# Kernel tuning notes

Hardware: AMD Instinct MI355X
Metric: run time of the kernel (lower is better)

## Reference

```python
import jax, jax.numpy as jnp
import numpy as np

DIM = 1536
NUM_HEADS = 16
HEAD_DIM = DIM // NUM_HEADS  # 96
ROPE_DIM = HEAD_DIM // 2     # 48
PT_SEQ = 32
FT_SEQ = 32
EPS = 1e-6


def _rope_tables():
    # VisionRotaryEmbedding(dim=48, pt_seq_len=32): 2D axial rotary tables
    f = 1.0 / (10000.0 ** (np.arange(0, ROPE_DIM, 2, dtype=np.float32)[: ROPE_DIM // 2] / ROPE_DIM))
    pos = np.arange(FT_SEQ, dtype=np.float32) / FT_SEQ * PT_SEQ
    freqs = pos[:, None] * f[None, :]                       # [32, 24]
    freqs = np.repeat(freqs, 2, axis=-1)                    # [32, 48] interleaved
    row = np.broadcast_to(freqs[:, None, :], (FT_SEQ, FT_SEQ, ROPE_DIM))
    col = np.broadcast_to(freqs[None, :, :], (FT_SEQ, FT_SEQ, ROPE_DIM))
    grid = np.concatenate([row, col], axis=-1).reshape(-1, HEAD_DIM)  # [1024, 96]
    return jnp.asarray(np.cos(grid)), jnp.asarray(np.sin(grid))


def _apply_rotary(x, cos, sin):
    # x: [B, S, H, D]; cos/sin: [S, D]; interleaved (use_real_unbind_dim=-1) rotation
    xr = x.reshape(*x.shape[:-1], -1, 2)
    x_rot = jnp.stack([-xr[..., 1], xr[..., 0]], axis=-1).reshape(x.shape)
    return x * cos[None, :, None, :] + x_rot * sin[None, :, None, :]


def _rms_norm(x, w):
    var = jnp.mean(jnp.square(x), axis=-1, keepdims=True)
    return x * jax.lax.rsqrt(var + EPS) * w


def setup_inputs() -> dict:
    key = jax.random.key(0)
    ks = jax.random.split(key, 12)
    s = 1.0 / np.sqrt(DIM)
    return {
        "hidden_states": jax.random.normal(ks[0], (8, 1024, DIM), dtype=jnp.float32),
        "Wq": jax.random.normal(ks[1], (DIM, DIM), dtype=jnp.float32) * s,
        "bq": jax.random.normal(ks[2], (DIM,), dtype=jnp.float32) * 0.01,
        "Wk": jax.random.normal(ks[3], (DIM, DIM), dtype=jnp.float32) * s,
        "bk": jax.random.normal(ks[4], (DIM,), dtype=jnp.float32) * 0.01,
        "Wv": jax.random.normal(ks[5], (DIM, DIM), dtype=jnp.float32) * s,
        "bv": jax.random.normal(ks[6], (DIM,), dtype=jnp.float32) * 0.01,
        "q_norm_w": jnp.ones((HEAD_DIM,), dtype=jnp.float32),
        "k_norm_w": jnp.ones((HEAD_DIM,), dtype=jnp.float32),
        "Wo": jax.random.normal(ks[7], (DIM, DIM), dtype=jnp.float32) * s,
        "bo": jax.random.normal(ks[8], (DIM,), dtype=jnp.float32) * 0.01,
    }


def reference(hidden_states, Wq, bq, Wk, bk, Wv, bv, q_norm_w, k_norm_w, Wo, bo):
    B, S, _ = hidden_states.shape
    cos, sin = _rope_tables()  # [S, HEAD_DIM], constants

    q = hidden_states @ Wq.T + bq
    k = hidden_states @ Wk.T + bk
    v = hidden_states @ Wv.T + bv
    q = q.reshape(B, S, NUM_HEADS, HEAD_DIM)
    k = k.reshape(B, S, NUM_HEADS, HEAD_DIM)
    v = v.reshape(B, S, NUM_HEADS, HEAD_DIM)

    q = _rms_norm(q, q_norm_w)
    k = _rms_norm(k, k_norm_w)
    q = _apply_rotary(q, cos, sin)
    k = _apply_rotary(k, cos, sin)

    scale = 1.0 / np.sqrt(HEAD_DIM)
    scores = jnp.einsum("bshd,bthd->bhst", q, k) * scale  # [B, H, S, S]
    probs = jax.nn.softmax(scores, axis=-1)
    out = jnp.einsum("bhst,bthd->bshd", probs, v)          # [B, S, H, D]
    out = out.reshape(B, S, DIM)
    return out @ Wo.T + bo
```

## Files before the change

kernel.cpp:

```cpp
#include <hip/hip_runtime.h>
#include <hip/hip_bf16.h>
#include <math.h>

typedef __hip_bfloat16 bf16;
typedef __attribute__((ext_vector_type(8))) short short8;
typedef __attribute__((ext_vector_type(4))) short short4v;
typedef __attribute__((ext_vector_type(4))) float f32x4;
typedef __attribute__((ext_vector_type(2))) int int2v;

#define MFMA16(a, b, c) __builtin_amdgcn_mfma_f32_16x16x32_bf16((a), (b), (c), 0, 0, 0)

typedef const __attribute__((address_space(1))) void GVOID;
typedef __attribute__((address_space(3))) void LVOID;

__device__ __forceinline__ float b2f(short s) {
    union { unsigned u; float f; } v;
    v.u = ((unsigned)(unsigned short)s) << 16;
    return v.f;
}
__device__ __forceinline__ short f2b(float f) {
    union { float f; unsigned u; } v;
    v.f = f;
    unsigned r = v.u + 0x7fffu + ((v.u >> 16) & 1u);
    return (short)(r >> 16);
}
__device__ __forceinline__ unsigned packbf2(float a, float b) {
    float2 t; t.x = a; t.y = b;
    __hip_bfloat162 h = __float22bfloat162_rn(t);
    union { __hip_bfloat162 h; unsigned u; } cv; cv.h = h;
    return cv.u;
}
__device__ __forceinline__ short bf2s(float x) {
    __hip_bfloat16 h = __float2bfloat16(x);
    union { __hip_bfloat16 h; short s; } cv; cv.h = h;
    return cv.s;
}

#if __has_builtin(__builtin_amdgcn_permlane32_swap)
__device__ __forceinline__ float addx32(float x) {
    union { float f; int i; } c; c.f = x;
    int2v r = __builtin_amdgcn_permlane32_swap(c.i, c.i, false, false);
    union { int i; float f; } a, b; a.i = r[0]; b.i = r[1];
    return a.f + b.f;
}
__device__ __forceinline__ float maxx32(float x) {
    union { float f; int i; } c; c.f = x;
    int2v r = __builtin_amdgcn_permlane32_swap(c.i, c.i, false, false);
    union { int i; float f; } a, b; a.i = r[0]; b.i = r[1];
    return fmaxf(a.f, b.f);
}
#else
__device__ __forceinline__ float addx32(float x) { return x + __shfl_xor(x, 32); }
__device__ __forceinline__ float maxx32(float x) { return fmaxf(x, __shfl_xor(x, 32)); }
#endif

#if __has_builtin(__builtin_amdgcn_permlane16_swap)
__device__ __forceinline__ float addx16(float x) {
    union { float f; int i; } c; c.f = x;
    int2v r = __builtin_amdgcn_permlane16_swap(c.i, c.i, false, false);
    union { int i; float f; } a, b; a.i = r[0]; b.i = r[1];
    return a.f + b.f;
}
__device__ __forceinline__ float maxx16(float x) {
    union { float f; int i; } c; c.f = x;
    int2v r = __builtin_amdgcn_permlane16_swap(c.i, c.i, false, false);
    union { int i; float f; } a, b; a.i = r[0]; b.i = r[1];
    return fmaxf(a.f, b.f);
}
#else
__device__ __forceinline__ float addx16(float x) { return x + __shfl_xor(x, 16); }
__device__ __forceinline__ float maxx16(float x) { return fmaxf(x, __shfl_xor(x, 16)); }
#endif

__global__ __launch_bounds__(256) void prep_kernel(
    const unsigned* __restrict__ X,
    const void* __restrict__ bq, const void* __restrict__ bk,
    const void* __restrict__ bv, const void* __restrict__ bo,
    const void* __restrict__ qw, const void* __restrict__ kw,
    int* __restrict__ flag, float* __restrict__ biasqkv, float* __restrict__ boc,
    float* __restrict__ qwc, float* __restrict__ kwc,
    float* __restrict__ cosT, float* __restrict__ sinT)
{
    const int tid = threadIdx.x;
    if (blockIdx.x == 0) {
        __shared__ int cnt;
        if (tid == 0) cnt = 0;
        __syncthreads();
        unsigned w = X[tid];
        unsigned e = (w >> 7) & 0xFFu;
        if (e > 140u) atomicAdd(&cnt, 1);
        __syncthreads();
        const int f = (cnt >= 16) ? 1 : 0;
        if (tid == 0) *flag = f;
        for (int i = tid; i < 6336; i += 256) {
            const void* src; float* dst; int j;
            if (i < 4608) {
                int m = i / 1536; j = i - m * 1536;
                src = (m == 0) ? bq : (m == 1) ? bk : bv; dst = biasqkv + i;
            } else if (i < 6144) { j = i - 4608; src = bo; dst = boc + j; }
            else if (i < 6240)   { j = i - 6144; src = qw; dst = qwc + j; }
            else                 { j = i - 6240; src = kw; dst = kwc + j; }
            *dst = f ? ((const float*)src)[j] : b2f(((const short*)src)[j]);
        }
    } else {
        int idx = (blockIdx.x - 1) * 256 + tid;
        if (idx >= 1024 * 96) return;
        int p = idx / 96;
        int d = idx - p * 96;
        int r = p >> 5, c = p & 31;
        int inRow = (d < 48);
        int dd = inRow ? d : d - 48;
        float pos = inRow ? (float)r : (float)c;
        float ex = -(float)(dd & ~1) / 48.0f;
        float f = powf(10000.0f, ex);
        float ang = pos * f;
        cosT[idx] = cosf(ang);
        sinT[idx] = sinf(ang);
    }
}

__device__ __forceinline__ void canon8(const void* src, short* dst, int i, int f) {
    short8 o;
    if (f) {
        const float* s = (const float*)src + (size_t)i * 8;
#pragma unroll
        for (int j = 0; j < 8; ++j) o[j] = f2b(s[j]);
    } else {
        o = ((const short8*)src)[i];
    }
    ((short8*)dst)[i] = o;
}

__global__ __launch_bounds__(256) void canon_all_kernel(
    const void* __restrict__ X,
    const void* __restrict__ s0, const void* __restrict__ s1,
    const void* __restrict__ s2, const void* __restrict__ s3,
    short* __restrict__ dX,
    short* __restrict__ d0, short* __restrict__ d1,
    short* __restrict__ d2, short* __restrict__ d3,
    const int* __restrict__ flag)
{
    const int f = *flag;
    const int bid = blockIdx.x;
    if (bid < 6144) {
        canon8(X, dX, bid * 256 + threadIdx.x, f);
    } else {
        const int wb = bid - 6144;
        const int m = wb / 1152;
        const int i = (wb - m * 1152) * 256 + threadIdx.x;
        const void* src = (m == 0) ? s0 : (m == 1) ? s1 : (m == 2) ? s2 : s3;
        short* dst = (m == 0) ? d0 : (m == 1) ? d1 : (m == 2) ? d2 : d3;
        canon8(src, dst, i, f);
    }
}

__global__ __launch_bounds__(256) void gemm128_kernel(
    const bf16* __restrict__ A, const bf16* __restrict__ Bw,
    const float* __restrict__ bias,
    bf16* __restrict__ O0, bf16* __restrict__ O1, bf16* __restrict__ O2,
    int K, const int* __restrict__ outFlag)
{
    __shared__ __align__(16) short As[2][128 * 64];
    __shared__ __align__(16) short Bs[2][128 * 64];

    const int tid = threadIdx.x;
    const int lane = tid & 63, w = tid >> 6;
    const int wr = w >> 1, wc = w & 1;
    const int li = lane & 15, lg = lane >> 4;

    const int pp = blockIdx.y * gridDim.x + blockIdx.x;
    const int xcd = pp & 7;
    const int idx = pp >> 3;
    const int mb = xcd * 8 + (idx & 7);
    const int nb = idx >> 3;
    const long mBase = (long)mb * 128;
    const long nGlob = (long)nb * 128;

    const bf16* aSrc[4]; const bf16* bSrc[4]; int ldsOff[4];
#pragma unroll
    for (int u = 0; u < 4; ++u) {
        const int L = u * 4096 + tid * 16;
        const int S = L ^ (((L >> 7) & 7) << 4);
        const int srow = S >> 7;
        const int scol = (S & 127) >> 1;
        aSrc[u] = A + (mBase + srow) * K + scol;
        bSrc[u] = Bw + (nGlob + srow) * K + scol;
        ldsOff[u] = L >> 1;
    }
    const int rxor = (li & 7) << 4;
    int kidx[2];
#pragma unroll
    for (int ks = 0; ks < 2; ++ks)
        kidx[ks] = ((ks * 64 + lg * 16) ^ rxor) >> 1;

    f32x4 acc[4][4] = {};
    const int NT = K >> 6;

    auto stage = [&](int tt, int bb) {
        const long kc = (long)tt * 64;
#pragma unroll
        for (int u = 0; u < 4; ++u)
            __builtin_amdgcn_global_load_lds((GVOID*)(aSrc[u] + kc),
                                             (LVOID*)&As[bb][ldsOff[u]], 16, 0, 0);
#pragma unroll
        for (int u = 0; u < 4; ++u)
            __builtin_amdgcn_global_load_lds((GVOID*)(bSrc[u] + kc),
                                             (LVOID*)&Bs[bb][ldsOff[u]], 16, 0, 0);
    };

    stage(0, 0);
    asm volatile("s_waitcnt vmcnt(0)" ::: "memory");
    __builtin_amdgcn_s_barrier();
    asm volatile("" ::: "memory");

    for (int t = 0; t < NT; ++t) {
        const int cb = t & 1;
        if (t + 1 < NT) stage(t + 1, cb ^ 1);
        const short* Ab = &As[cb][0];
        const short* Bb = &Bs[cb][0];
#pragma unroll
        for (int ks = 0; ks < 2; ++ks) {
            short8 fa[4], fb[4];
#pragma unroll
            for (int m = 0; m < 4; ++m)
                fa[m] = *(const short8*)(Ab + (wr * 64 + m * 16 + li) * 64 + kidx[ks]);
#pragma unroll
            for (int n = 0; n < 4; ++n)
                fb[n] = *(const short8*)(Bb + (wc * 64 + n * 16 + li) * 64 + kidx[ks]);
            __builtin_amdgcn_sched_barrier(0);
            __builtin_amdgcn_s_setprio(1);
#pragma unroll
            for (int m = 0; m < 4; ++m)
#pragma unroll
                for (int n = 0; n < 4; ++n)
                    acc[m][n] = MFMA16(fa[m], fb[n], acc[m][n]);
            __builtin_amdgcn_s_setprio(0);
            __builtin_amdgcn_sched_barrier(0);
        }
        asm volatile("s_waitcnt vmcnt(0)" ::: "memory");
        __builtin_amdgcn_s_barrier();
        asm volatile("" ::: "memory");
    }

    const int f32out = outFlag ? *outFlag : 0;
    const int mat = nb / 12;
    const long colBase = nGlob - (long)mat * 1536;
    bf16* Ob = (mat == 0) ? O0 : (mat == 1) ? O1 : O2;
    if (f32out) {
        float* Cf = (float*)Ob;
#pragma unroll
        for (int n = 0; n < 4; ++n) {
            const long col = colBase + wc * 64 + n * 16 + li;
            const float bv = bias[nGlob + wc * 64 + n * 16 + li];
#pragma unroll
            for (int m = 0; m < 4; ++m) {
                const long row = mBase + wr * 64 + m * 16 + lg * 4;
#pragma unroll
                for (int i = 0; i < 4; ++i)
                    Cf[(row + i) * 1536 + col] = acc[m][n][i] + bv;
            }
        }
    } else {
#pragma unroll
        for (int n = 0; n < 4; ++n) {
            const long col = colBase + wc * 64 + n * 16 + li;
            const float bv = bias[nGlob + wc * 64 + n * 16 + li];
#pragma unroll
            for (int m = 0; m < 4; ++m) {
                const long row = mBase + wr * 64 + m * 16 + lg * 4;
#pragma unroll
                for (int i = 0; i < 4; ++i)
                    Ob[(row + i) * 1536 + col] = __float2bfloat16(acc[m][n][i] + bv);
            }
        }
    }
}

__global__ __launch_bounds__(256) void norm_rope2_kernel(
    bf16* __restrict__ Qb, bf16* __restrict__ Kb,
    const float* __restrict__ qwc, const float* __restrict__ kwc,
    const float* __restrict__ cosT, const float* __restrict__ sinT,
    float qscale)
{
    bf16* T = blockIdx.y ? Kb : Qb;
    const float* wgt = blockIdx.y ? kwc : qwc;
    const float scale = blockIdx.y ? 1.0f : qscale;

    const int row = blockIdx.x * 256 + threadIdx.x;
    const int tok = row >> 4;
    const int h = row & 15;
    const int spos = tok & 1023;
    bf16* p = T + (size_t)tok * 1536 + h * 96;

    float x[96];
#pragma unroll
    for (int v = 0; v < 12; ++v) {
        short8 t = *(const short8*)(p + v * 8);
#pragma unroll
        for (int j = 0; j < 8; ++j) x[v * 8 + j] = b2f(t[j]);
    }
    float ss = 0.f;
#pragma unroll
    for (int d = 0; d < 96; ++d) ss += x[d] * x[d];
    const float rn = scale / sqrtf(ss * (1.0f / 96.0f) + 1e-6f);

    const float* cr = cosT + spos * 96;
    const float* sr = sinT + spos * 96;

#pragma unroll
    for (int v = 0; v < 12; ++v) {
        short8 o;
#pragma unroll
        for (int j = 0; j < 8; j += 2) {
            const int d = v * 8 + j;
            const float x0 = x[d] * rn * wgt[d];
            const float x1 = x[d + 1] * rn * wgt[d + 1];
            o[j]     = f2b(x0 * cr[d] - x1 * sr[d]);
            o[j + 1] = f2b(x1 * cr[d + 1] + x0 * sr[d + 1]);
        }
        *(short8*)(p + v * 8) = o;
    }
}

__global__ __launch_bounds__(512, 2) void attn_kernel(
    const bf16* __restrict__ Q, const bf16* __restrict__ K,
    const bf16* __restrict__ V, bf16* __restrict__ O)
{
    __shared__ __align__(16) short Ks[2][64 * 96];
    __shared__ __align__(16) short Vt[2][96 * 64];

    const int tid = threadIdx.x;
    const int l = tid & 63, w = tid >> 6;
    const int li = l & 15, lg = l >> 4;

    const int p = blockIdx.x;
    const int lb = (p & 7) * 128 + (p >> 3);
    const int qt = lb & 7;
    const int bh = lb >> 3;
    const int b = bh >> 4, h = bh & 15;
    const size_t tokBase = (size_t)b * 1024;

    short8 aq[3];
    {
        const bf16* qp = Q + (tokBase + qt * 128 + w * 16 + li) * 1536 + h * 96;
#pragma unroll
        for (int kk = 0; kk < 3; ++kk)
            aq[kk] = *(const short8*)(qp + kk * 32 + lg * 8);
    }

    float m_r = -1e30f, l_r = 0.f;
    f32x4 o[6] = {};

    const bool kst = (w >= 4);
    int kr[3], km[3], kso[3];
#pragma unroll
    for (int u = 0; u < 3; ++u) {
        const int c = (tid - 256) + 256 * u;
        const int crr = c / 12;
        kr[u] = crr;
        km[u] = (c - crr * 12) * 8;
        kso[u] = (crr * 96 + km[u]) ^ ((crr & 7) << 3);
    }
    const int t2 = tid >> 3;
    const int dh = tid & 7;
    const bf16* vbase = V + (tokBase + 2 * t2) * 1536 + h * 96 + dh * 12;

    const int rowbase = ((li >> 2) << 3) + (li & 3);
    const int colb = lg * 8;
    int frow[2][2];
    int fswz[2];
#pragma unroll
    for (int kt = 0; kt < 2; ++kt)
#pragma unroll
        for (int hh = 0; hh < 2; ++hh)
            frow[kt][hh] = (kt * 32 + 4 * hh + rowbase) * 96;
#pragma unroll
    for (int hh = 0; hh < 2; ++hh)
        fswz[hh] = (4 * hh + (li & 3)) << 3;

    const int vswz = ((li >> 1) & 7) << 3;

    short8 kreg[3];
    short4v vr0[3], vr1[3];
    auto loadT = [&](int tt) {
        if (kst) {
#pragma unroll
            for (int u = 0; u < 3; ++u)
                kreg[u] = *(const short8*)(K + (tokBase + tt + kr[u]) * 1536 + h * 96 + km[u]);
        } else {
            const bf16* vp = vbase + (size_t)tt * 1536;
#pragma unroll
            for (int u = 0; u < 3; ++u) {
                vr0[u] = *(const short4v*)(vp + u * 4);
                vr1[u] = *(const short4v*)(vp + 1536 + u * 4);
            }
        }
    };
    auto writeT = [&](int bb) {
        if (kst) {
#pragma unroll
            for (int u = 0; u < 3; ++u)
                *(short8*)&Ks[bb][kso[u]] = kreg[u];
        } else {
            unsigned* Vt32 = (unsigned*)&Vt[bb][0];
#pragma unroll
            for (int u = 0; u < 3; ++u)
#pragma unroll
                for (int j = 0; j < 4; ++j) {
                    const int d = dh * 12 + u * 4 + j;
                    const unsigned pk = ((unsigned)(unsigned short)vr0[u][j]) |
                                        (((unsigned)(unsigned short)vr1[u][j]) << 16);
                    Vt32[(d * 32 + t2) ^ (((d >> 1) & 7) << 2)] = pk;
                }
        }
    };

    loadT(0);
    writeT(0);
    loadT(64);
    __syncthreads();

    for (int t = 0; t < 16; ++t) {
        const int cb = t & 1;

        f32x4 s4[4] = {};
#pragma unroll
        for (int kk = 0; kk < 3; ++kk) {
            const int ck = kk * 32 + colb;
#pragma unroll
            for (int kt = 0; kt < 2; ++kt)
#pragma unroll
                for (int hh = 0; hh < 2; ++hh) {
                    short8 fk = *(const short8*)&Ks[cb][(frow[kt][hh] + ck) ^ fswz[hh]];
                    s4[kt * 2 + hh] = MFMA16(fk, aq[kk], s4[kt * 2 + hh]);
                }
        }

        if (t < 15) writeT(cb ^ 1);
        if (t < 14) loadT((t + 2) * 64);

        unsigned pdw[4][2];
        {
            float mk[4];
#pragma unroll
            for (int kn = 0; kn < 4; ++kn)
                mk[kn] = fmaxf(fmaxf(s4[kn][0], s4[kn][1]),
                               fmaxf(s4[kn][2], s4[kn][3]));
            float pm = fmaxf(fmaxf(mk[0], mk[1]), fmaxf(mk[2], mk[3]));
            pm = maxx16(pm);
            pm = maxx32(pm);

            float alpha = 1.0f;
            const bool need = (pm > m_r + 8.0f);
            if (need) { alpha = exp2f(m_r - pm); m_r = pm; }
            const float mn = m_r;

            float rs = 0.f;
#pragma unroll
            for (int kn = 0; kn < 4; ++kn) {
                float p0 = exp2f(s4[kn][0] - mn);
                float p1 = exp2f(s4[kn][1] - mn);
                float p2 = exp2f(s4[kn][2] - mn);
                float p3 = exp2f(s4[kn][3] - mn);
                rs += (p0 + p1) + (p2 + p3);
                pdw[kn][0] = packbf2(p0, p1);
                pdw[kn][1] = packbf2(p2, p3);
            }
            rs = addx16(rs);
            rs = addx32(rs);
            l_r = l_r * alpha + rs;
            if (need) {
#pragma unroll
                for (int dn = 0; dn < 6; ++dn)
#pragma unroll
                    for (int i = 0; i < 4; ++i) o[dn][i] *= alpha;
            }
        }

#pragma unroll
        for (int kt = 0; kt < 2; ++kt) {
            union { unsigned u[4]; short8 s; } pa;
            pa.u[0] = pdw[kt * 2][0];
            pa.u[1] = pdw[kt * 2][1];
            pa.u[2] = pdw[kt * 2 + 1][0];
            pa.u[3] = pdw[kt * 2 + 1][1];
#pragma unroll
            for (int dn = 0; dn < 6; ++dn) {
                short8 fv = *(const short8*)&Vt[cb][((dn * 16 + li) * 64 + kt * 32 + lg * 8) ^ vswz];
                o[dn] = MFMA16(fv, pa.s, o[dn]);
            }
        }

        __syncthreads();
    }

    {
        const float inv = 1.0f / l_r;
        const size_t row = tokBase + qt * 128 + w * 16 + li;
#pragma unroll
        for (int dn = 0; dn < 6; ++dn) {
            short4v ov;
#pragma unroll
            for (int i = 0; i < 4; ++i) ov[i] = bf2s(o[dn][i] * inv);
            *(short4v*)&O[row * 1536 + h * 96 + dn * 16 + lg * 4] = ov;
        }
    }
}

extern "C" void kernel_launch(void* const* d_in, const int* in_sizes, int n_in,
                              void* d_out, int out_size, void* d_ws, size_t ws_size,
                              hipStream_t stream) {
    const void* X  = d_in[0];
    const void* Wq = d_in[1];
    const void* bq = d_in[2];
    const void* Wk = d_in[3];
    const void* bk = d_in[4];
    const void* Wv = d_in[5];
    const void* bv = d_in[6];
    const void* qw = d_in[7];
    const void* kw = d_in[8];
    const void* Wo = d_in[9];
    const void* bo = d_in[10];

    char* ws = (char*)d_ws;
    size_t off = 0;
    int* flag = (int*)ws;                      off += 256;
    float* cosT = (float*)(ws + off);          off += 1024 * 96 * 4;
    float* sinT = (float*)(ws + off);          off += 1024 * 96 * 4;
    float* biasqkv = (float*)(ws + off);       off += 4608 * 4;
    float* boc  = (float*)(ws + off);          off += 1536 * 4;
    float* qwc  = (float*)(ws + off);          off += 128 * 4;
    float* kwc  = (float*)(ws + off);          off += 128 * 4;
    off = (off + 255) & ~(size_t)255;
    bf16* Wc  = (bf16*)(ws + off);             off += (size_t)4608 * 1536 * 2;
    bf16* Woc = (bf16*)(ws + off);             off += (size_t)1536 * 1536 * 2;
    bf16* Xc  = (bf16*)(ws + off);             off += (size_t)8192 * 1536 * 2;
    bf16* Qb  = (bf16*)(ws + off);             off += (size_t)8192 * 1536 * 2;
    bf16* Kb  = (bf16*)(ws + off);             off += (size_t)8192 * 1536 * 2;
    bf16* Vb  = (bf16*)(ws + off);             off += (size_t)8192 * 1536 * 2;
    bf16* AO  = Xc;

    prep_kernel<<<385, 256, 0, stream>>>((const unsigned*)X, bq, bk, bv, bo, qw, kw,
                                         flag, biasqkv, boc, qwc, kwc, cosT, sinT);

    canon_all_kernel<<<10752, 256, 0, stream>>>(
        X, Wq, Wk, Wv, Wo,
        (short*)Xc, (short*)Wc, (short*)(Wc + (size_t)1536 * 1536),
        (short*)(Wc + (size_t)2 * 1536 * 1536), (short*)Woc, flag);

    gemm128_kernel<<<dim3(36, 64), 256, 0, stream>>>(
        Xc, Wc, biasqkv, Qb, Kb, Vb, 1536, nullptr);

    const float qscale = (float)(0.10206207261596577 * 1.4426950408889634);
    norm_rope2_kernel<<<dim3(512, 2), 256, 0, stream>>>(Qb, Kb, qwc, kwc, cosT, sinT, qscale);

    attn_kernel<<<1024, 512, 0, stream>>>(Qb, Kb, Vb, AO);

    gemm128_kernel<<<dim3(12, 64), 256, 0, stream>>>(
        AO, Woc, boc, (bf16*)d_out, (bf16*)d_out, (bf16*)d_out, 1536, flag);
}
```

Before: 378.6 us.

## Use 256x256-tile 8-wave ping-pong GEMM for fused QKV projection

Adds a new QKV projection GEMM that uses 256x256 output tiles with 512 threads (8 waves). It splits the A and B LDS buffers into halves so loads of the next K-tile are interleaved across eight barrier-separated MFMA phases. The larger tile cuts global and LDS traffic per FLOP and improves overlap of loads with MFMA, at the cost of higher register pressure, a grid of only 576 blocks, and many extra barriers. The output-projection GEMM keeps the old kernel, simplified to a single output pointer.

```diff
diff --git a/kernel.cpp b/kernel.cpp
--- a/kernel.cpp
+++ b/kernel.cpp
@@ -154,10 +154,167 @@
     }
 }
 
-__global__ __launch_bounds__(256) void gemm128_kernel(
+__global__ __launch_bounds__(512, 2) void gemm8p_kernel(
     const bf16* __restrict__ A, const bf16* __restrict__ Bw,
     const float* __restrict__ bias,
     bf16* __restrict__ O0, bf16* __restrict__ O1, bf16* __restrict__ O2,
+    int K, const int* __restrict__ outFlag)
+{
+    __shared__ __align__(16) short As[2][2][8192];
+    __shared__ __align__(16) short Bs[2][2][8192];
+
+    const int tid = threadIdx.x;
+    const int lane = tid & 63, w = tid >> 6;
+    const int wm = w >> 2, wn = w & 3;
+    const int li = lane & 15, lg = lane >> 4;
+    const int hbx = wn >> 1;
+    const int rb0 = (wn & 1) * 64;
+
+    const int pp = blockIdx.y * gridDim.x + blockIdx.x;
+    const int xcd = pp & 7;
+    const int idx = pp >> 3;
+    const int mb = xcd * 4 + (idx & 3);
+    const int nb = idx >> 2;
+    const long mBase = (long)mb * 256;
+    const long nGlob = (long)nb * 256;
+
+    int srowL[2], scolL[2], ldso[2];
+#pragma unroll
+    for (int u = 0; u < 2; ++u) {
+        const int L = u * 8192 + tid * 16;
+        const int S = L ^ (((L >> 7) & 7) << 4);
+        srowL[u] = S >> 7;
+        scolL[u] = (S & 127) >> 1;
+        ldso[u] = L >> 1;
+    }
+    const int rxor = (li & 7) << 4;
+    int koff[2];
+#pragma unroll
+    for (int ks = 0; ks < 2; ++ks)
+        koff[ks] = ((ks * 64 + lg * 16) ^ rxor) >> 1;
+
+    f32x4 acc[8][4] = {};
+    const int NT = K >> 6;
+
+    auto stageA = [&](int t, int h) {
+        const long kc = (long)t * 64;
+#pragma unroll
+        for (int u = 0; u < 2; ++u)
+            __builtin_amdgcn_global_load_lds(
+                (GVOID*)(A + (mBase + h * 128 + srowL[u]) * K + kc + scolL[u]),
+                (LVOID*)&As[t & 1][h][ldso[u]], 16, 0, 0);
+    };
+    auto stageB = [&](int t, int h) {
+        const long kc = (long)t * 64;
+#pragma unroll
+        for (int u = 0; u < 2; ++u)
+            __builtin_amdgcn_global_load_lds(
+                (GVOID*)(Bw + (nGlob + h * 128 + srowL[u]) * K + kc + scolL[u]),
+                (LVOID*)&Bs[t & 1][h][ldso[u]], 16, 0, 0);
+    };
+
+    short8 fa[4][2], fb[2][2];
+    auto readFA = [&](int buf, int qm) {
+#pragma unroll
+        for (int m = 0; m < 4; ++m) {
+            const int r = qm * 64 + m * 16 + li;
+#pragma unroll
+            for (int ks = 0; ks < 2; ++ks)
+                fa[m][ks] = *(const short8*)&As[buf][wm][r * 64 + koff[ks]];
+        }
+    };
+    auto readFB = [&](int buf, int qn) {
+#pragma unroll
+        for (int n = 0; n < 2; ++n) {
+            const int r = rb0 + qn * 32 + n * 16 + li;
+#pragma unroll
+            for (int ks = 0; ks < 2; ++ks)
+                fb[n][ks] = *(const short8*)&Bs[buf][hbx][r * 64 + koff[ks]];
+        }
+    };
+    auto mfmaPh = [&](int qm, int qn) {
+        __builtin_amdgcn_s_setprio(1);
+#pragma unroll
+        for (int m = 0; m < 4; ++m)
+#pragma unroll
+            for (int n = 0; n < 2; ++n)
+#pragma unroll
+                for (int ks = 0; ks < 2; ++ks)
+                    acc[qm * 4 + m][qn * 2 + n] =
+                        MFMA16(fa[m][ks], fb[n][ks], acc[qm * 4 + m][qn * 2 + n]);
+        __builtin_amdgcn_s_setprio(0);
+    };
+
+#define PH_SYNC1() do { __builtin_amdgcn_s_barrier(); \
+    asm volatile("s_waitcnt lgkmcnt(0)" ::: "memory"); \
+    __builtin_amdgcn_sched_barrier(0); } while (0)
+#define PH_SYNC2() do { __builtin_amdgcn_sched_barrier(0); \
+    __builtin_amdgcn_s_barrier(); } while (0)
+#define PH_SYNC2V() do { __builtin_amdgcn_sched_barrier(0); \
+    asm volatile("s_waitcnt vmcnt(2)" ::: "memory"); \
+    __builtin_amdgcn_s_barrier(); } while (0)
+
+    stageA(0, 0); stageA(0, 1); stageB(0, 0); stageB(0, 1); stageA(1, 0);
+    asm volatile("s_waitcnt vmcnt(2)" ::: "memory");
+    __builtin_amdgcn_s_barrier();
+
+    for (int j = 0; j < NT / 2; ++j) {
+        const int t1 = 2 * j + 1, t2 = 2 * j + 2, t3 = 2 * j + 3;
+        readFA(0, 0); readFB(0, 0); stageA(t1, 1);
+        PH_SYNC1(); mfmaPh(0, 0); PH_SYNC2();
+        readFB(0, 1); stageB(t1, 0);
+        PH_SYNC1(); mfmaPh(0, 1); PH_SYNC2();
+        readFA(0, 1); readFB(0, 0); stageB(t1, 1);
+        PH_SYNC1(); mfmaPh(1, 0); PH_SYNC2();
+        readFB(0, 1); if (t2 < NT) stageA(t2, 0);
+        PH_SYNC1(); mfmaPh(1, 1); PH_SYNC2V();
+        readFA(1, 0); readFB(1, 0); if (t2 < NT) stageA(t2, 1);
+        PH_SYNC1(); mfmaPh(0, 0); PH_SYNC2();
+        readFB(1, 1); if (t2 < NT) stageB(t2, 0);
+        PH_SYNC1(); mfmaPh(0, 1); PH_SYNC2();
+        readFA(1, 1); readFB(1, 0); if (t2 < NT) stageB(t2, 1);
+        PH_SYNC1(); mfmaPh(1, 0); PH_SYNC2();
+        readFB(1, 1); if (t3 < NT) stageA(t3, 0);
+        PH_SYNC1(); mfmaPh(1, 1); PH_SYNC2V();
+    }
+
+    const int f32out = outFlag ? *outFlag : 0;
+    const int mat = nb / 6;
+    const long colBase = nGlob - (long)mat * 1536;
+    bf16* Ob = (mat == 0) ? O0 : (mat == 1) ? O1 : O2;
+    if (f32out) {
+        float* Cf = (float*)Ob;
+#pragma unroll
+        for (int n = 0; n < 4; ++n) {
+            const long col = colBase + wn * 64 + n * 16 + li;
+            const float bv = bias[nGlob + wn * 64 + n * 16 + li];
+#pragma unroll
+            for (int m = 0; m < 8; ++m) {
+                const long row = mBase + wm * 128 + m * 16 + lg * 4;
+#pragma unroll
+                for (int i = 0; i < 4; ++i)
+                    Cf[(row + i) * 1536 + col] = acc[m][n][i] + bv;
+            }
+        }
+    } else {
+#pragma unroll
+        for (int n = 0; n < 4; ++n) {
+            const long col = colBase + wn * 64 + n * 16 + li;
+            const float bv = bias[nGlob + wn * 64 + n * 16 + li];
+#pragma unroll
+            for (int m = 0; m < 8; ++m) {
+                const long row = mBase + wm * 128 + m * 16 + lg * 4;
+#pragma unroll
+                for (int i = 0; i < 4; ++i)
+                    Ob[(row + i) * 1536 + col] = __float2bfloat16(acc[m][n][i] + bv);
+            }
+        }
+    }
+}
+
+__global__ __launch_bounds__(256) void gemm128_kernel(
+    const bf16* __restrict__ A, const bf16* __restrict__ Bw,
+    const float* __restrict__ bias, void* __restrict__ C,
     int K, const int* __restrict__ outFlag)
 {
     __shared__ __align__(16) short As[2][128 * 64];
@@ -174,7 +331,7 @@
     const int mb = xcd * 8 + (idx & 7);
     const int nb = idx >> 3;
     const long mBase = (long)mb * 128;
-    const long nGlob = (long)nb * 128;
+    const long nBase = (long)nb * 128;
 
     const bf16* aSrc[4]; const bf16* bSrc[4]; int ldsOff[4];
 #pragma unroll
@@ -184,7 +341,7 @@
         const int srow = S >> 7;
         const int scol = (S & 127) >> 1;
         aSrc[u] = A + (mBase + srow) * K + scol;
-        bSrc[u] = Bw + (nGlob + srow) * K + scol;
+        bSrc[u] = Bw + (nBase + srow) * K + scol;
         ldsOff[u] = L >> 1;
     }
     const int rxor = (li & 7) << 4;
@@ -243,15 +400,12 @@
     }
 
     const int f32out = outFlag ? *outFlag : 0;
-    const int mat = nb / 12;
-    const long colBase = nGlob - (long)mat * 1536;
-    bf16* Ob = (mat == 0) ? O0 : (mat == 1) ? O1 : O2;
     if (f32out) {
-        float* Cf = (float*)Ob;
+        float* Cf = (float*)C;
 #pragma unroll
         for (int n = 0; n < 4; ++n) {
-            const long col = colBase + wc * 64 + n * 16 + li;
-            const float bv = bias[nGlob + wc * 64 + n * 16 + li];
+            const long col = nBase + wc * 64 + n * 16 + li;
+            const float bv = bias[col];
 #pragma unroll
             for (int m = 0; m < 4; ++m) {
                 const long row = mBase + wr * 64 + m * 16 + lg * 4;
@@ -261,16 +415,17 @@
             }
         }
     } else {
+        bf16* Cb = (bf16*)C;
 #pragma unroll
         for (int n = 0; n < 4; ++n) {
-            const long col = colBase + wc * 64 + n * 16 + li;
-            const float bv = bias[nGlob + wc * 64 + n * 16 + li];
+            const long col = nBase + wc * 64 + n * 16 + li;
+            const float bv = bias[col];
 #pragma unroll
             for (int m = 0; m < 4; ++m) {
                 const long row = mBase + wr * 64 + m * 16 + lg * 4;
 #pragma unroll
                 for (int i = 0; i < 4; ++i)
-                    Ob[(row + i) * 1536 + col] = __float2bfloat16(acc[m][n][i] + bv);
+                    Cb[(row + i) * 1536 + col] = __float2bfloat16(acc[m][n][i] + bv);
             }
         }
     }
@@ -548,7 +703,7 @@
         (short*)Xc, (short*)Wc, (short*)(Wc + (size_t)1536 * 1536),
         (short*)(Wc + (size_t)2 * 1536 * 1536), (short*)Woc, flag);
 
-    gemm128_kernel<<<dim3(36, 64), 256, 0, stream>>>(
+    gemm8p_kernel<<<dim3(18, 32), 512, 0, stream>>>(
         Xc, Wc, biasqkv, Qb, Kb, Vb, 1536, nullptr);
 
     const float qscale = (float)(0.10206207261596577 * 1.4426950408889634);
@@ -557,5 +712,5 @@
     attn_kernel<<<1024, 512, 0, stream>>>(Qb, Kb, Vb, AO);
 
     gemm128_kernel<<<dim3(12, 64), 256, 0, stream>>>(
-        AO, Woc, boc, (bf16*)d_out, (bf16*)d_out, (bf16*)d_out, 1536, flag);
-}
+        AO, Woc, boc, (bf16*)d_out, 1536, flag);
+}
```

Result: no change. 381.1 us (+0.7%).
